# Kernel tuning notes

Hardware: AMD Instinct MI355X
Metric: run time of the kernel (lower is better)

Reference implementation:

```python
import jax, jax.numpy as jnp
import numpy as np

B, S, IN_DIM, P_DIM, H = 2, 2048, 1024, 512, 8
HD = P_DIM // H
N_PENTA = 1024
SCALES = (128, 256, 512)
K_NEIGH = max(16, min(int(S * 0.15), 128))  # adaptive window -> 128
SCALE = 1.0 / float(np.sqrt(HD))
EPS = 1e-5


def _ln(x, g, b):
    mu = jnp.mean(x, axis=-1, keepdims=True)
    var = jnp.mean((x - mu) ** 2, axis=-1, keepdims=True)
    return (x - mu) * jax.lax.rsqrt(var + EPS) * g + b


def setup_inputs() -> dict:
    key = jax.random.key(0)
    ks = list(jax.random.split(key, 6 + 2 * len(SCALES)))
    w = lambda k, shp: jax.random.normal(k, shp, jnp.float32) * 0.02
    inp = {
        'sequence_features': jax.random.normal(ks[0], (B, S, IN_DIM), jnp.float32),
        'shared_pentachora': jax.random.normal(ks[1], (N_PENTA, 5, P_DIM), jnp.float32),
        'shared_positions': jax.random.uniform(ks[2], (N_PENTA,), dtype=jnp.float32),
        'proj_W': w(ks[3], (IN_DIM, P_DIM)), 'proj_b': jnp.zeros((P_DIM,), jnp.float32),
        'ln_g': jnp.ones((P_DIM,), jnp.float32), 'ln_b': jnp.zeros((P_DIM,), jnp.float32),
        'qkv_W': w(ks[4], (P_DIM, 3 * P_DIM)), 'qkv_b': jnp.zeros((3 * P_DIM,), jnp.float32),
        'out_W': w(ks[5], (P_DIM, P_DIM)), 'out_b': jnp.zeros((P_DIM,), jnp.float32),
    }
    i = 6
    for s in SCALES:
        inp[f'w1_{s}'] = w(ks[i], (P_DIM, 2 * s)); inp[f'b1_{s}'] = jnp.zeros((2 * s,), jnp.float32)
        inp[f'g_{s}'] = jnp.ones((2 * s,), jnp.float32); inp[f'bb_{s}'] = jnp.zeros((2 * s,), jnp.float32)
        inp[f'w2_{s}'] = w(ks[i + 1], (2 * s, s)); inp[f'b2_{s}'] = jnp.zeros((s,), jnp.float32)
        i += 2
    return inp


def _attend_one(z_b, pos_b, qkv_W, qkv_b, out_W, out_b):
    # z_b: [S, P_DIM], pos_b: [S]
    qkv = (z_b @ qkv_W + qkv_b).reshape(S, 3, H, HD)
    q = jnp.transpose(qkv[:, 0], (1, 0, 2))  # [H, S, HD]
    k = jnp.transpose(qkv[:, 1], (1, 0, 2))
    v = jnp.transpose(qkv[:, 2], (1, 0, 2))
    dist = jnp.abs(pos_b[:, None] - pos_b[None, :])  # [S, S]
    _, routes = jax.lax.top_k(-dist, K_NEIGH)        # [S, K] nearest in Cantor space
    kg = k[:, routes, :]  # [H, S, K, HD] gathered keys
    vg = v[:, routes, :]
    scores = jnp.einsum('hqd,hqkd->hqk', q, kg) * SCALE
    attn = jax.nn.softmax(scores, axis=-1)
    out = jnp.einsum('hqk,hqkd->hqd', attn, vg)
    out = jnp.transpose(out, (1, 0, 2)).reshape(S, P_DIM)
    return out @ out_W + out_b


def reference(sequence_features, shared_pentachora, shared_positions, proj_W, proj_b, ln_g, ln_b, qkv_W, qkv_b, out_W, out_b, w1_128, b1_128, g_128, bb_128, w2_128, b2_128, w1_256, b1_256, g_256, bb_256, w2_256, b2_256, w1_512, b1_512, g_512, bb_512, w2_512, b2_512):
    # centroids from pentachora vertices, L2-normalized
    cent = shared_pentachora.mean(axis=1)
    cent = cent / jnp.clip(jnp.linalg.norm(cent, axis=-1, keepdims=True), 1e-12)
    # input projection -> LN -> GELU -> L2 normalize
    z = jax.nn.gelu(_ln(sequence_features @ proj_W + proj_b, ln_g, ln_b), approximate=False)
    z = z / jnp.clip(jnp.linalg.norm(z, axis=-1, keepdims=True), 1e-12)
    # match to opinion anchors, inherit Cantor positions
    anchor_ids = jnp.argmax(jnp.einsum('bnd,pd->bnp', z, cent), axis=-1)  # [B, S]
    cantor_positions = shared_positions[anchor_ids]  # [B, S]
    # per-sample geometric sparse attention (vmapped over batch)
    z_att = jax.vmap(_attend_one, in_axes=(0, 0, None, None, None, None))(
        z, cantor_positions, qkv_W, qkv_b, out_W, out_b)  # [B, S, P_DIM]
    pooled = z_att.mean(axis=1)  # [B, P_DIM] (no attention mask)
    scale_params = (
        (w1_128, b1_128, g_128, bb_128, w2_128, b2_128),
        (w1_256, b1_256, g_256, bb_256, w2_256, b2_256),
        (w1_512, b1_512, g_512, bb_512, w2_512, b2_512),
    )
    outs = []
    for (w1, b1, g, bb, w2, b2) in scale_params:
        h = jax.nn.gelu(_ln(pooled @ w1 + b1, g, bb), approximate=False)
        outs.append(h @ w2 + b2)
    return jnp.concatenate(outs, axis=-1)  # [B, 128+256+512] concatenated scale opinions
```

## Files before the change

### kernel.cpp

```cpp
#include <hip/hip_runtime.h>
#include <math.h>

#define DEV __device__ __forceinline__

static constexpr int S_LEN  = 2048;
static constexpr int IN_DIM = 1024;
static constexpr int P_DIM  = 512;
static constexpr int NHEAD  = 8;
static constexpr int HD     = 64;
static constexpr int KN     = 128;

typedef __attribute__((ext_vector_type(8))) short bf16x8;
typedef __attribute__((ext_vector_type(4))) float f32x4;

DEV float gelu_exact(float x) {
    return 0.5f * x * (1.0f + erff(x * 0.70710678118654752440f));
}

DEV short bf_hi(float x) {
    unsigned u = __float_as_uint(x);
    unsigned r = (u + 0x7fffu + ((u >> 16) & 1u)) >> 16;
    return (short)r;
}
DEV float bf_f(short h) { return __uint_as_float(((unsigned)(unsigned short)h) << 16); }

DEV float block_reduce_sum(float v, float* sm4) {
    #pragma unroll
    for (int off = 32; off; off >>= 1) v += __shfl_down(v, off, 64);
    int lane = threadIdx.x & 63, w = threadIdx.x >> 6;
    __syncthreads();
    if (lane == 0) sm4[w] = v;
    __syncthreads();
    return sm4[0] + sm4[1] + sm4[2] + sm4[3];
}

__global__ __launch_bounds__(256) void k_cent(const float* __restrict__ penta,
                                              short* __restrict__ ch,
                                              short* __restrict__ cl) {
    int p = blockIdx.x, t = threadIdx.x;
    __shared__ float sm4[4];
    float c0 = 0.f, c1 = 0.f;
    #pragma unroll
    for (int v = 0; v < 5; v++) {
        const float* row = penta + ((long)p * 5 + v) * P_DIM;
        c0 += row[t];
        c1 += row[t + 256];
    }
    c0 /= 5.0f; c1 /= 5.0f;
    float tot = block_reduce_sum(c0 * c0 + c1 * c1, sm4);
    float n = fmaxf(sqrtf(tot), 1e-12f);
    float v0 = c0 / n, v1 = c1 / n;
    short h0 = bf_hi(v0), h1 = bf_hi(v1);
    ch[p * P_DIM + t]       = h0;
    ch[p * P_DIM + t + 256] = h1;
    cl[p * P_DIM + t]       = bf_hi(v0 - bf_f(h0));
    cl[p * P_DIM + t + 256] = bf_hi(v1 - bf_f(h1));
}

template <int K, int N>
__global__ __launch_bounds__(256) void k_wt(const float* __restrict__ W,
                                            short* __restrict__ WTh,
                                            short* __restrict__ WTl) {
    __shared__ float tile[64][65];
    int bk = blockIdx.x, bn = blockIdx.y;
    int t = threadIdx.x;
    int c = t & 63, r4 = t >> 6;
    #pragma unroll
    for (int i = 0; i < 16; i++) {
        int row = r4 + i * 4;
        tile[row][c] = W[(long)(bk * 64 + row) * N + bn * 64 + c];
    }
    __syncthreads();
    #pragma unroll
    for (int i = 0; i < 16; i++) {
        int n = r4 + i * 4;
        float v = tile[c][n];
        short h = bf_hi(v);
        long o = (long)(bn * 64 + n) * K + bk * 64 + c;
        WTh[o] = h;
        WTl[o] = bf_hi(v - bf_f(h));
    }
}

template <int BM, int K, int N, int EPI, bool SPLITA>
__global__ __launch_bounds__(256) void k_mm(const float* __restrict__ Af,
                                            const short* __restrict__ Ash,
                                            const short* __restrict__ Asl,
                                            const short* __restrict__ BTh,
                                            const short* __restrict__ BTl,
                                            const float* __restrict__ bias,
                                            float* __restrict__ C,
                                            unsigned long long* __restrict__ rowkey) {
    constexpr int TI = BM / 32;
    __shared__ short Ah[BM * 40], Al[BM * 40], Bh[128 * 40], Bl[128 * 40];
    int t = threadIdx.x;
    int lane = t & 63, wave = t >> 6;
    int wr = (wave >> 1) * (BM / 2), wc = (wave & 1) * 64;
    int m = lane & 15, quad = lane >> 4;
    int rb = blockIdx.x * BM, cb = blockIdx.y * 128;

    f32x4 acc[TI][4];
    #pragma unroll
    for (int i = 0; i < TI; i++)
        #pragma unroll
        for (int j = 0; j < 4; j++) acc[i][j] = (f32x4){0.f, 0.f, 0.f, 0.f};

    for (int k0 = 0; k0 < K; k0 += 32) {
        __syncthreads();
        if constexpr (SPLITA) {
            #pragma unroll
            for (int ps = 0; ps < BM / 64; ps++) {
                int idx = t + ps * 256;
                int row = idx >> 2, c4 = idx & 3;
                *(float4*)(Ah + row * 40 + c4 * 8) =
                    *(const float4*)(Ash + (long)(rb + row) * K + k0 + c4 * 8);
                *(float4*)(Al + row * 40 + c4 * 8) =
                    *(const float4*)(Asl + (long)(rb + row) * K + k0 + c4 * 8);
            }
        } else {
            #pragma unroll
            for (int ps = 0; ps < BM / 32; ps++) {
                int row = (t >> 3) + ps * 32;
                int seg = t & 7;
                float4 v = *(const float4*)(Af + (long)(rb + row) * K + k0 + seg * 4);
                short h0 = bf_hi(v.x), h1 = bf_hi(v.y), h2 = bf_hi(v.z), h3 = bf_hi(v.w);
                short l0 = bf_hi(v.x - bf_f(h0)), l1 = bf_hi(v.y - bf_f(h1));
                short l2 = bf_hi(v.z - bf_f(h2)), l3 = bf_hi(v.w - bf_f(h3));
                *(short4*)(Ah + row * 40 + seg * 4) = make_short4(h0, h1, h2, h3);
                *(short4*)(Al + row * 40 + seg * 4) = make_short4(l0, l1, l2, l3);
            }
        }
        #pragma unroll
        for (int ps = 0; ps < 2; ps++) {
            int row = (t >> 2) + ps * 64;
            int seg = t & 3;
            *(float4*)(Bh + row * 40 + seg * 8) =
                *(const float4*)(BTh + (long)(cb + row) * K + k0 + seg * 8);
            *(float4*)(Bl + row * 40 + seg * 8) =
                *(const float4*)(BTl + (long)(cb + row) * K + k0 + seg * 8);
        }
        __syncthreads();

        bf16x8 ah[TI], al[TI], bh[4], bl[4];
        #pragma unroll
        for (int i = 0; i < TI; i++) {
            ah[i] = *(const bf16x8*)(Ah + (wr + i * 16 + m) * 40 + quad * 8);
            al[i] = *(const bf16x8*)(Al + (wr + i * 16 + m) * 40 + quad * 8);
        }
        #pragma unroll
        for (int j = 0; j < 4; j++) {
            bh[j] = *(const bf16x8*)(Bh + (wc + j * 16 + m) * 40 + quad * 8);
            bl[j] = *(const bf16x8*)(Bl + (wc + j * 16 + m) * 40 + quad * 8);
        }
        #pragma unroll
        for (int i = 0; i < TI; i++)
            #pragma unroll
            for (int j = 0; j < 4; j++) {
                acc[i][j] = __builtin_amdgcn_mfma_f32_16x16x32_bf16(ah[i], bh[j], acc[i][j], 0, 0, 0);
                acc[i][j] = __builtin_amdgcn_mfma_f32_16x16x32_bf16(ah[i], bl[j], acc[i][j], 0, 0, 0);
                acc[i][j] = __builtin_amdgcn_mfma_f32_16x16x32_bf16(al[i], bh[j], acc[i][j], 0, 0, 0);
            }
    }

    if (EPI == 0) {
        #pragma unroll
        for (int i = 0; i < TI; i++) {
            int gr0 = rb + wr + i * 16 + quad * 4;
            #pragma unroll
            for (int j = 0; j < 4; j++) {
                int gc = cb + wc + j * 16 + m;
                float bv = bias[gc];
                #pragma unroll
                for (int r = 0; r < 4; r++)
                    C[(long)(gr0 + r) * N + gc] = acc[i][j][r] + bv;
            }
        }
    } else {
        #pragma unroll
        for (int i = 0; i < TI; i++) {
            #pragma unroll
            for (int r = 0; r < 4; r++) {
                int gr = rb + wr + i * 16 + quad * 4 + r;
                float bv = acc[i][0][r];
                int bp = cb + wc + m;
                #pragma unroll
                for (int j = 1; j < 4; j++) {
                    float v = acc[i][j][r];
                    int p = cb + wc + j * 16 + m;
                    if (v > bv) { bv = v; bp = p; }
                }
                #pragma unroll
                for (int off = 1; off < 16; off <<= 1) {
                    float ov = __shfl_xor(bv, off, 64);
                    int op = __shfl_xor(bp, off, 64);
                    if (ov > bv || (ov == bv && op < bp)) { bv = ov; bp = op; }
                }
                if (m == 0) {
                    unsigned u = __float_as_uint(bv);
                    u = (u & 0x80000000u) ? ~u : (u | 0x80000000u);
                    unsigned long long key =
                        ((unsigned long long)u << 32) | (unsigned)(0xFFFFFFFFu - (unsigned)bp);
                    atomicMax(&rowkey[gr], key);
                }
            }
        }
    }
}

__global__ __launch_bounds__(256) void k_ln_gelu_norm(const float* __restrict__ Zin,
                                                      const float* __restrict__ g,
                                                      const float* __restrict__ b,
                                                      short* __restrict__ z_h,
                                                      short* __restrict__ z_l) {
    long row = blockIdx.x;
    int t = threadIdx.x;
    __shared__ float sm4[4];
    float x0 = Zin[row * P_DIM + t], x1 = Zin[row * P_DIM + t + 256];
    float mu = block_reduce_sum(x0 + x1, sm4) * (1.0f / P_DIM);
    float d0 = x0 - mu, d1 = x1 - mu;
    float var = block_reduce_sum(d0 * d0 + d1 * d1, sm4) * (1.0f / P_DIM);
    float rs = 1.0f / sqrtf(var + 1e-5f);
    float y0 = gelu_exact(d0 * rs * g[t] + b[t]);
    float y1 = gelu_exact(d1 * rs * g[t + 256] + b[t + 256]);
    float nn = block_reduce_sum(y0 * y0 + y1 * y1, sm4);
    float n = fmaxf(sqrtf(nn), 1e-12f);
    float v0 = y0 / n, v1 = y1 / n;
    short h0 = bf_hi(v0), h1 = bf_hi(v1);
    z_h[row * P_DIM + t]       = h0;
    z_h[row * P_DIM + t + 256] = h1;
    z_l[row * P_DIM + t]       = bf_hi(v0 - bf_f(h0));
    z_l[row * P_DIM + t + 256] = bf_hi(v1 - bf_f(h1));
}

__global__ __launch_bounds__(256) void k_sort(const unsigned long long* __restrict__ rowkey,
                                              const float* __restrict__ spos,
                                              int* __restrict__ order,
                                              float* __restrict__ pos_srt) {
    int b = blockIdx.x, t = threadIdx.x;
    __shared__ unsigned long long key[2048];
    for (int u = 0; u < 8; u++) {
        int i = t + u * 256;
        unsigned p = 0xFFFFFFFFu - (unsigned)(rowkey[b * 2048 + i] & 0xFFFFFFFFull);
        float pv = spos[p];
        key[i] = (((unsigned long long)__float_as_uint(pv)) << 32) | (unsigned)i;
    }
    __syncthreads();
    for (int k = 2; k <= 2048; k <<= 1) {
        for (int j = k >> 1; j > 0; j >>= 1) {
            for (int u = 0; u < 8; u++) {
                int i = t + u * 256;
                int l = i ^ j;
                if (l > i) {
                    bool up = ((i & k) == 0);
                    unsigned long long a = key[i], c = key[l];
                    if ((a > c) == up) { key[i] = c; key[l] = a; }
                }
            }
            __syncthreads();
        }
    }
    for (int u = 0; u < 8; u++) {
        int r = t + u * 256;
        unsigned long long kk = key[r];
        order[b * 2048 + r]   = (int)(kk & 0xffffffffu);
        pos_srt[b * 2048 + r] = __uint_as_float((unsigned)(kk >> 32));
    }
}

__global__ __launch_bounds__(256) void k_routes(const float* __restrict__ pos_srt,
                                                const int* __restrict__ order,
                                                unsigned long long* __restrict__ bmG,
                                                uint2* __restrict__ bounds) {
    int blk = blockIdx.x;
    int b = blk >> 9;
    int t = threadIdx.x;
    int lane = t & 63, wave = t >> 6;
    int r = (blk & 511) * 4 + wave;
    __shared__ float ps[2048];
    __shared__ unsigned short tk[2048];
    for (int u = 0; u < 8; u++) {
        int i = t + u * 256;
        ps[i] = pos_srt[b * 2048 + i];
        tk[i] = (unsigned short)order[b * 2048 + i];
    }
    __syncthreads();

    float pi = ps[r];
    float T = 3e38f;
    #pragma unroll
    for (int a2 = 0; a2 < 2; a2++) {
        int a = lane + a2 * 64;
        int jl = r - a, jr = r + 127 - a;
        if (jl >= 0 && jr <= 2047) {
            float dl = (a > 0)   ? (pi - ps[jl]) : 0.f;
            float dr = (a < 127) ? (ps[jr] - pi) : 0.f;
            T = fminf(T, fmaxf(dl, dr));
        }
    }
    #pragma unroll
    for (int off = 1; off < 64; off <<= 1) T = fminf(T, __shfl_xor(T, off, 64));

    int lo = 0, hi = r;
    while (lo < hi) { int mid = (lo + hi) >> 1; if (pi - ps[mid] <= T) hi = mid; else lo = mid + 1; }
    int mn = lo;
    lo = r; hi = 2047;
    while (lo < hi) { int mid = (lo + hi + 1) >> 1; if (ps[mid] - pi <= T) lo = mid; else hi = mid - 1; }
    int mx = lo;
    int Ls, Rs;
    if (T > 0.f) {
        lo = 0; hi = r;
        while (lo < hi) { int mid = (lo + hi) >> 1; if (pi - ps[mid] < T) hi = mid; else lo = mid + 1; }
        Ls = lo;
        lo = r; hi = 2047;
        while (lo < hi) { int mid = (lo + hi + 1) >> 1; if (ps[mid] - pi < T) lo = mid; else hi = mid - 1; }
        Rs = lo;
    } else { Ls = r + 1; Rs = r - 1; }

    int cnt_strict = (Rs >= Ls) ? (Rs - Ls + 1) : 0;
    int need = 128 - cnt_strict;
    int l0a, l0b, r0a, r0b;
    if (cnt_strict > 0) { l0a = mn; l0b = Ls - 1; r0a = Rs + 1; r0b = mx; }
    else                { l0a = mn; l0b = mx;     r0a = 1;      r0b = 0; }
    int nL = (l0b >= l0a) ? (l0b - l0a + 1) : 0;
    int nR = (r0b >= r0a) ? (r0b - r0a + 1) : 0;
    int tiecount = nL + nR;

    int X = 65535;
    if (need < tiecount) {
        int lo2 = 0, hi2 = 2047;
        while (lo2 < hi2) {
            int mid = (lo2 + hi2) >> 1;
            int cnt = 0;
            for (int e = lane; e < tiecount; e += 64) {
                int j = (e < nL) ? (l0a + e) : (r0a + e - nL);
                cnt += (tk[j] <= mid) ? 1 : 0;
            }
            #pragma unroll
            for (int off = 1; off < 64; off <<= 1) cnt += __shfl_xor(cnt, off, 64);
            if (cnt >= need) hi2 = mid; else lo2 = mid + 1;
        }
        X = lo2;
    }

    int qlo_loc = 1 << 30, qhi_loc = -1;
    if (lane < 32) {
        unsigned long long bits = 0;
        int j0 = lane << 6, j1 = j0 + 63;
        if (cnt_strict > 0) {
            int a0 = max(Ls, j0), a1 = min(Rs, j1);
            if (a0 <= a1) {
                int s = a0 - j0, e = a1 - j0;
                unsigned long long msk = (e - s == 63) ? ~0ull
                                       : (((1ull << (e - s + 1)) - 1) << s);
                bits |= msk;
            }
        }
        int a0 = max(l0a, j0), a1 = min(l0b, j1);
        for (int j = a0; j <= a1; j++) if (tk[j] <= X) bits |= 1ull << (j - j0);
        a0 = max(r0a, j0); a1 = min(r0b, j1);
        for (int j = a0; j <= a1; j++) if (tk[j] <= X) bits |= 1ull << (j - j0);
        if (bits) {
            qlo_loc = j0 + __builtin_ctzll(bits);
            qhi_loc = j0 + 63 - __builtin_clzll(bits);
        }
        bmG[((long)(b * 2048 + r)) * 32 + lane] = bits;
    }
    #pragma unroll
    for (int off = 1; off < 64; off <<= 1) {
        qlo_loc = min(qlo_loc, __shfl_xor(qlo_loc, off, 64));
        qhi_loc = max(qhi_loc, __shfl_xor(qhi_loc, off, 64));
    }
    if (lane == 0)
        bounds[b * 2048 + r] = make_uint2((unsigned)qlo_loc, (unsigned)qhi_loc);
}

__global__ __launch_bounds__(256) void k_kprep(const float* __restrict__ qkv,
                                               const int* __restrict__ order,
                                               short* __restrict__ Ks_h,
                                               short* __restrict__ Ks_l) {
    int b = blockIdx.y;
    int t = threadIdx.x;
    int lr = t >> 5;
    int seg = t & 31;
    int rank = blockIdx.x * 8 + lr;
    int tok = order[b * 2048 + rank];
    const float4* src = (const float4*)qkv + (long)(b * 2048 + tok) * 384 + 128 + seg * 4;
    long dsto = (long)(b * 2048 + rank) * 512 + seg * 16;
    #pragma unroll
    for (int u = 0; u < 4; u++) {
        float4 v = src[u];
        short h0 = bf_hi(v.x), h1 = bf_hi(v.y), h2 = bf_hi(v.z), h3 = bf_hi(v.w);
        *(short4*)(Ks_h + dsto + u * 4) = make_short4(h0, h1, h2, h3);
        *(short4*)(Ks_l + dsto + u * 4) =
            make_short4(bf_hi(v.x - bf_f(h0)), bf_hi(v.y - bf_f(h1)),
                        bf_hi(v.z - bf_f(h2)), bf_hi(v.w - bf_f(h3)));
    }
}

__global__ __launch_bounds__(256) void k_vprep(const float* __restrict__ qkv,
                                               const int* __restrict__ order,
                                               short* __restrict__ Vt_h) {
    __shared__ short tile[64][72];
    int rt = blockIdx.x, dt = blockIdx.y, b = blockIdx.z;
    int t = threadIdx.x;
    int lr = t >> 2;
    int q4 = t & 3;
    int tok = order[b * 2048 + rt * 64 + lr];
    const float4* src = (const float4*)qkv + (long)(b * 2048 + tok) * 384 + 256 + dt * 16;
    #pragma unroll
    for (int u = 0; u < 4; u++) {
        float4 v = src[q4 + u * 4];
        int d0 = (q4 + u * 4) * 4;
        tile[d0 + 0][lr] = bf_hi(v.x);
        tile[d0 + 1][lr] = bf_hi(v.y);
        tile[d0 + 2][lr] = bf_hi(v.z);
        tile[d0 + 3][lr] = bf_hi(v.w);
    }
    __syncthreads();
    int d = t >> 2, c4 = t & 3;
    long o = ((long)(b * 512 + dt * 64 + d)) * 2048 + rt * 64 + c4 * 16;
    #pragma unroll
    for (int j = 0; j < 4; j++)
        *(short4*)(Vt_h + o + j * 4) = make_short4(tile[d][c4 * 16 + j * 4 + 0],
                                                   tile[d][c4 * 16 + j * 4 + 1],
                                                   tile[d][c4 * 16 + j * 4 + 2],
                                                   tile[d][c4 * 16 + j * 4 + 3]);
}

__global__ __launch_bounds__(256) void k_attn(const float* __restrict__ qkv,
                                              const int* __restrict__ order,
                                              const unsigned long long* __restrict__ bmG,
                                              const uint2* __restrict__ bounds,
                                              const short* __restrict__ Ks_h,
                                              const short* __restrict__ Ks_l,
                                              const short* __restrict__ Vt_h,
                                              short* __restrict__ attn_h,
                                              short* __restrict__ attn_l) {
    __shared__ __align__(16) char smem[17024];
    short* Pt = (short*)smem;
    unsigned short* cm = (unsigned short*)(smem + 10240);
    float* Opart = (float*)smem;
    float2* ml = (float2*)(smem + 16384);
    int* sh_tok = (int*)(smem + 16896);
    int* sh_lohi = (int*)(smem + 16960);

    int gb = blockIdx.x;
    int b  = gb >> 9;
    int qg = (gb >> 2) & 127;
    int hp = gb & 3;
    int h0 = hp * 2;
    int r0 = qg * 16;
    int t = threadIdx.x;
    int lane = t & 63, wave = t >> 6;
    int rh = wave & 1, hs = wave >> 1;
    int key = lane & 15, quad = lane >> 4;

    const float4* qkvF4 = (const float4*)qkv;

    if (t < 16) sh_tok[t] = order[b * 2048 + r0 + t];
    if (t == 0) { sh_lohi[0] = 1 << 30; sh_lohi[1] = 0; }
    #pragma unroll
    for (int u = 0; u < 8; u++) {
        int e = t + u * 256;
        int c = e >> 4, q = e & 15;
        cm[c * 16 + q] = (unsigned short)(
            (bmG[((long)(b * 2048 + r0 + q)) * 32 + (c >> 2)] >> ((c & 3) * 16)) & 0xFFFF);
    }
    __syncthreads();
    if (t < 16) {
        uint2 bd = bounds[b * 2048 + r0 + t];
        atomicMin(&sh_lohi[0], (int)bd.x);
        atomicMax(&sh_lohi[1], (int)bd.y);
    }

    bf16x8 qh[2], ql[2];
    {
        long tq = (long)(b * 2048 + sh_tok[key]) * 384;
        #pragma unroll
        for (int ks = 0; ks < 2; ks++) {
            float4 v0 = qkvF4[tq + (h0 + hs) * 16 + ks * 8 + quad * 2];
            float4 v1 = qkvF4[tq + (h0 + hs) * 16 + ks * 8 + quad * 2 + 1];
            float vv[8] = {v0.x, v0.y, v0.z, v0.w, v1.x, v1.y, v1.z, v1.w};
            #pragma unroll
            for (int j = 0; j < 8; j++) {
                short hb = bf_hi(vv[j]);
                qh[ks][j] = hb;
                ql[ks][j] = bf_hi(vv[j] - bf_f(hb));
            }
        }
    }
    __syncthreads();
    int lo = sh_lohi[0] & ~63, hi = sh_lohi[1] + 1;

    float mrow[4], lrow[4];
    f32x4 Ont[4];
    #pragma unroll
    for (int r = 0; r < 4; r++) { mrow[r] = -1e30f; lrow[r] = 0.f; }
    #pragma unroll
    for (int nt = 0; nt < 4; nt++) Ont[nt] = (f32x4){0.f, 0.f, 0.f, 0.f};

    short* PtH = Pt + wave * 1280;
    short* PtL = PtH + 640;

    int hd = h0 + hs;
    long kbase = ((long)b * 2048) * 512 + hd * 64 + quad * 8;
    long vbase = ((long)(b * 512 + hd * 64 + key)) * 2048;

    for (int c0 = lo; c0 < hi; c0 += 64) {
        int cb = c0 + rh * 32;
        if (cb >= hi) continue;
        int ch0 = cb >> 4;
        unsigned long long m0 = *(const unsigned long long*)(cm + ch0 * 16 + quad * 4);
        unsigned long long m1 = (ch0 + 1 < 128)
            ? *(const unsigned long long*)(cm + (ch0 + 1) * 16 + quad * 4) : 0ull;
        if (!__any((m0 | m1) != 0ull)) continue;

        long kr0 = kbase + (long)(cb + key) * 512;
        long kr1 = kbase + (long)(cb + 16 + key) * 512;

        f32x4 S0 = (f32x4){0.f,0.f,0.f,0.f}, S1 = (f32x4){0.f,0.f,0.f,0.f};
        #pragma unroll
        for (int ks = 0; ks < 2; ks++) {
            bf16x8 b0h = *(const bf16x8*)(Ks_h + kr0 + ks * 32);
            bf16x8 b0l = *(const bf16x8*)(Ks_l + kr0 + ks * 32);
            bf16x8 b1h = *(const bf16x8*)(Ks_h + kr1 + ks * 32);
            bf16x8 b1l = *(const bf16x8*)(Ks_l + kr1 + ks * 32);
            S0 = __builtin_amdgcn_mfma_f32_16x16x32_bf16(qh[ks], b0h, S0, 0, 0, 0);
            S0 = __builtin_amdgcn_mfma_f32_16x16x32_bf16(qh[ks], b0l, S0, 0, 0, 0);
            S0 = __builtin_amdgcn_mfma_f32_16x16x32_bf16(ql[ks], b0h, S0, 0, 0, 0);
            S1 = __builtin_amdgcn_mfma_f32_16x16x32_bf16(qh[ks], b1h, S1, 0, 0, 0);
            S1 = __builtin_amdgcn_mfma_f32_16x16x32_bf16(qh[ks], b1l, S1, 0, 0, 0);
            S1 = __builtin_amdgcn_mfma_f32_16x16x32_bf16(ql[ks], b1h, S1, 0, 0, 0);
        }
        float s0[4], s1[4], p0[4], p1[4];
        unsigned bit0[4], bit1[4];
        #pragma unroll
        for (int r = 0; r < 4; r++) {
            bit0[r] = (unsigned)((m0 >> (r * 16 + key)) & 1);
            bit1[r] = (unsigned)((m1 >> (r * 16 + key)) & 1);
            s0[r] = bit0[r] ? S0[r] * 0.125f : -1e30f;
            s1[r] = bit1[r] ? S1[r] * 0.125f : -1e30f;
        }
        #pragma unroll
        for (int r = 0; r < 4; r++) {
            float cmax = fmaxf(s0[r], s1[r]);
            cmax = fmaxf(cmax, __shfl_xor(cmax, 1, 64));
            cmax = fmaxf(cmax, __shfl_xor(cmax, 2, 64));
            cmax = fmaxf(cmax, __shfl_xor(cmax, 4, 64));
            cmax = fmaxf(cmax, __shfl_xor(cmax, 8, 64));
            float mn = fmaxf(mrow[r], cmax);
            float alpha = __expf(mrow[r] - mn);
            mrow[r] = mn;
            p0[r] = bit0[r] ? __expf(s0[r] - mn) : 0.f;
            p1[r] = bit1[r] ? __expf(s1[r] - mn) : 0.f;
            float rs = p0[r] + p1[r];
            rs += __shfl_xor(rs, 1, 64);
            rs += __shfl_xor(rs, 2, 64);
            rs += __shfl_xor(rs, 4, 64);
            rs += __shfl_xor(rs, 8, 64);
            lrow[r] = lrow[r] * alpha + rs;
            #pragma unroll
            for (int nt = 0; nt < 4; nt++) Ont[nt][r] *= alpha;
        }
        #pragma unroll
        for (int r = 0; r < 4; r++) {
            short ha = bf_hi(p0[r]);
            PtH[(quad * 4 + r) * 40 + key] = ha;
            PtL[(quad * 4 + r) * 40 + key] = bf_hi(p0[r] - bf_f(ha));
            short hb = bf_hi(p1[r]);
            PtH[(quad * 4 + r) * 40 + 16 + key] = hb;
            PtL[(quad * 4 + r) * 40 + 16 + key] = bf_hi(p1[r] - bf_f(hb));
        }
        bf16x8 pfh = *(const bf16x8*)(PtH + key * 40 + quad * 8);
        bf16x8 pfl = *(const bf16x8*)(PtL + key * 40 + quad * 8);
        #pragma unroll
        for (int nt = 0; nt < 4; nt++) {
            bf16x8 vf = *(const bf16x8*)(Vt_h + vbase + (long)nt * 16 * 2048
                                         + cb + quad * 8);
            Ont[nt] = __builtin_amdgcn_mfma_f32_16x16x32_bf16(pfh, vf, Ont[nt], 0, 0, 0);
            Ont[nt] = __builtin_amdgcn_mfma_f32_16x16x32_bf16(pfl, vf, Ont[nt], 0, 0, 0);
        }
    }

    if (key == 0) {
        #pragma unroll
        for (int r = 0; r < 4; r++)
            ml[(rh * 2 + hs) * 16 + quad * 4 + r] = make_float2(mrow[r], lrow[r]);
    }
    __syncthreads();
    #pragma unroll
    for (int nt = 0; nt < 4; nt++)
        #pragma unroll
        for (int r = 0; r < 4; r++)
            Opart[rh * 2048 + (quad * 4 + r) * 128 + hs * 64 + nt * 16 + key] = Ont[nt][r];
    __syncthreads();

    {
        int q = t >> 4, hs2 = (t >> 3) & 1, ds = t & 7;
        float2 a = ml[(0 * 2 + hs2) * 16 + q];
        float2 c = ml[(1 * 2 + hs2) * 16 + q];
        float M = fmaxf(a.x, c.x);
        float w0 = __expf(a.x - M), w1 = __expf(c.x - M);
        float denom = a.y * w0 + c.y * w1;
        float inv = 1.0f / fmaxf(denom, 1e-37f);
        long off = (long)(b * 2048 + sh_tok[q]) * P_DIM + (h0 + hs2) * HD + ds * 8;
        short hsv[8], lsv[8];
        #pragma unroll
        for (int j = 0; j < 8; j++) {
            int d = hs2 * 64 + ds * 8 + j;
            float o = (Opart[q * 128 + d] * w0 + Opart[2048 + q * 128 + d] * w1) * inv;
            hsv[j] = bf_hi(o);
            lsv[j] = bf_hi(o - bf_f(hsv[j]));
        }
        *(short4*)(attn_h + off)     = make_short4(hsv[0], hsv[1], hsv[2], hsv[3]);
        *(short4*)(attn_h + off + 4) = make_short4(hsv[4], hsv[5], hsv[6], hsv[7]);
        *(short4*)(attn_l + off)     = make_short4(lsv[0], lsv[1], lsv[2], lsv[3]);
        *(short4*)(attn_l + off + 4) = make_short4(lsv[4], lsv[5], lsv[6], lsv[7]);
    }
}

__global__ __launch_bounds__(256) void k_pool(const float* __restrict__ zatt,
                                              float* __restrict__ pooled) {
    int b = blockIdx.y, chunk = blockIdx.x, t = threadIdx.x;
    float a0 = 0.f, a1 = 0.f;
    for (int s = 0; s < 16; s++) {
        long row = ((long)b * S_LEN + chunk * 16 + s) * P_DIM;
        a0 += zatt[row + t];
        a1 += zatt[row + t + 256];
    }
    atomicAdd(&pooled[b * P_DIM + t], a0);
    atomicAdd(&pooled[b * P_DIM + t + 256], a1);
}

__global__ __launch_bounds__(256) void k_exp_fc1(const float* __restrict__ pooled,
                                                 const float* __restrict__ w1_0, const float* __restrict__ b1_0,
                                                 const float* __restrict__ w1_1, const float* __restrict__ b1_1,
                                                 const float* __restrict__ w1_2, const float* __restrict__ b1_2,
                                                 float* __restrict__ h) {
    int t = threadIdx.x, b = blockIdx.y;
    int c = blockIdx.x * 256 + t;
    __shared__ float pl[P_DIM];
    pl[t]       = pooled[b * P_DIM + t]       * (1.0f / S_LEN);
    pl[t + 256] = pooled[b * P_DIM + t + 256] * (1.0f / S_LEN);
    __syncthreads();

    const float* wp; const float* bp; int s2, j;
    if (c < 256)      { wp = w1_0; bp = b1_0; s2 = 256;  j = c; }
    else if (c < 768) { wp = w1_1; bp = b1_1; s2 = 512;  j = c - 256; }
    else              { wp = w1_2; bp = b1_2; s2 = 1024; j = c - 768; }

    const float* p = wp + j;
    float acc = 0.f;
    #pragma unroll 16
    for (int k = 0; k < P_DIM; k++) {
        acc = fmaf(pl[k], *p, acc);
        p += s2;
    }
    h[(long)b * 1792 + c] = acc + bp[j];
}

__global__ __launch_bounds__(256) void k_exp_ln(float* __restrict__ h,
                                                const float* __restrict__ g0, const float* __restrict__ bb0,
                                                const float* __restrict__ g1, const float* __restrict__ bb1,
                                                const float* __restrict__ g2, const float* __restrict__ bb2) {
    int e = blockIdx.x, b = blockIdx.y, t = threadIdx.x;
    __shared__ float sm4[4];
    const int offs[3] = {0, 256, 768};
    const int ns[3]   = {256, 512, 1024};
    const float* gs[3]  = {g0, g1, g2};
    const float* bbs[3] = {bb0, bb1, bb2};
    int n = ns[e];
    float* hp = h + (long)b * 1792 + offs[e];
    const float* g = gs[e]; const float* bb = bbs[e];

    float x[4];
    float loc = 0.f;
    for (int u = 0; u < 4; u++) {
        int j = t + u * 256;
        x[u] = (j < n) ? hp[j] : 0.f;
        loc += x[u];
    }
    float mu = block_reduce_sum(loc, sm4) / (float)n;
    loc = 0.f;
    for (int u = 0; u < 4; u++) {
        int j = t + u * 256;
        if (j < n) { float d = x[u] - mu; loc += d * d; }
    }
    float var = block_reduce_sum(loc, sm4) / (float)n;
    float rs = 1.0f / sqrtf(var + 1e-5f);
    for (int u = 0; u < 4; u++) {
        int j = t + u * 256;
        if (j < n) hp[j] = gelu_exact((x[u] - mu) * rs * g[j] + bb[j]);
    }
}

__global__ __launch_bounds__(256) void k_exp_fc2(const float* __restrict__ h,
                                                 const float* __restrict__ w2_0, const float* __restrict__ b2_0,
                                                 const float* __restrict__ w2_1, const float* __restrict__ b2_1,
                                                 const float* __restrict__ w2_2, const float* __restrict__ b2_2,
                                                 float* __restrict__ out) {
    int t = threadIdx.x, b = blockIdx.y;
    int c = blockIdx.x * 256 + t;
    __shared__ float hs[1792];
    for (int u = 0; u < 7; u++) hs[t + u * 256] = h[(long)b * 1792 + t + u * 256];
    __syncthreads();
    if (c >= 896) return;

    const float* wp; const float* bp; int s2, sN, j, off_h;
    if (c < 128)      { wp = w2_0; bp = b2_0; s2 = 256;  sN = 128; j = c;       off_h = 0; }
    else if (c < 384) { wp = w2_1; bp = b2_1; s2 = 512;  sN = 256; j = c - 128; off_h = 256; }
    else              { wp = w2_2; bp = b2_2; s2 = 1024; sN = 512; j = c - 384; off_h = 768; }

    const float* p = wp + j;
    const float* hh = hs + off_h;
    float acc = 0.f;
    #pragma unroll 16
    for (int k = 0; k < s2; k++) {
        acc = fmaf(hh[k], *p, acc);
        p += sN;
    }
    out[b * 896 + c] = acc + bp[j];
}

extern "C" void kernel_launch(void* const* d_in, const int* in_sizes, int n_in,
                              void* d_out, int out_size, void* d_ws, size_t ws_size,
                              hipStream_t stream) {
    const float* seq   = (const float*)d_in[0];
    const float* penta = (const float*)d_in[1];
    const float* spos  = (const float*)d_in[2];
    const float* projW = (const float*)d_in[3];
    const float* projb = (const float*)d_in[4];
    const float* lng   = (const float*)d_in[5];
    const float* lnb   = (const float*)d_in[6];
    const float* qkvW  = (const float*)d_in[7];
    const float* qkvb  = (const float*)d_in[8];
    const float* outW  = (const float*)d_in[9];
    const float* outb  = (const float*)d_in[10];

    float* ws      = (float*)d_ws;
    float* z_pre   = ws;
    short* z_h     = (short*)(z_pre + 2097152);
    short* z_l     = z_h + 2097152;
    float* qkv     = (float*)(z_l + 2097152);
    float* pos     = qkv + 6291456;
    float* pooled  = pos + 4096;
    float* hbuf    = pooled + 1024;
    unsigned long long* rowkey = (unsigned long long*)(hbuf + 4096);
    float* pos_srt = (float*)(rowkey + 4096);
    int*   order   = (int*)(pos_srt + 4096);
    uint2* bounds  = (uint2*)(order + 4096);
    unsigned long long* bmG = (unsigned long long*)(bounds + 4096);
    short* cent_h  = (short*)(bmG + 131072);
    short* cent_l  = cent_h + 524288;
    short* pjWT_h  = cent_l + 524288;
    short* pjWT_l  = pjWT_h + 524288;
    short* qkWT_h  = pjWT_l + 524288;
    short* qkWT_l  = qkWT_h + 786432;
    short* owWT_h  = qkWT_l + 786432;
    short* owWT_l  = owWT_h + 262144;
    short* attn_h  = z_h;
    short* attn_l  = z_l;
    float* zatt    = z_pre;

    short* Ks_h = (short*)z_pre;
    short* Ks_l = Ks_h + 2097152;
    short* Vt_h = cent_h;

    k_cent<<<1024, 256, 0, stream>>>(penta, cent_h, cent_l);
    { dim3 g(16, 8);  k_wt<IN_DIM, P_DIM><<<g, 256, 0, stream>>>(projW, pjWT_h, pjWT_l); }
    { dim3 g(8, 24);  k_wt<P_DIM, 3 * P_DIM><<<g, 256, 0, stream>>>(qkvW, qkWT_h, qkWT_l); }
    { dim3 g(8, 8);   k_wt<P_DIM, P_DIM><<<g, 256, 0, stream>>>(outW, owWT_h, owWT_l); }

    { dim3 g(64, 4);  k_mm<64, IN_DIM, P_DIM, 0, false><<<g, 256, 0, stream>>>(
          seq, nullptr, nullptr, pjWT_h, pjWT_l, projb, z_pre, nullptr); }
    k_ln_gelu_norm<<<4096, 256, 0, stream>>>(z_pre, lng, lnb, z_h, z_l);

    hipMemsetAsync(rowkey, 0, 4096 * sizeof(unsigned long long), stream);
    { dim3 g(64, 8);  k_mm<64, P_DIM, 1024, 1, true><<<g, 256, 0, stream>>>(
          nullptr, z_h, z_l, cent_h, cent_l, nullptr, nullptr, rowkey); }
    k_sort<<<2, 256, 0, stream>>>(rowkey, spos, order, pos_srt);

    { dim3 g(64, 12); k_mm<64, P_DIM, 3 * P_DIM, 0, true><<<g, 256, 0, stream>>>(
          nullptr, z_h, z_l, qkWT_h, qkWT_l, qkvb, qkv, nullptr); }
    k_routes<<<1024, 256, 0, stream>>>(pos_srt, order, bmG, bounds);
    { dim3 g(256, 2); k_kprep<<<g, 256, 0, stream>>>(qkv, order, Ks_h, Ks_l); }
    { dim3 g(32, 8, 2); k_vprep<<<g, 256, 0, stream>>>(qkv, order, Vt_h); }
    k_attn<<<1024, 256, 0, stream>>>(qkv, order, bmG, bounds,
                                     Ks_h, Ks_l, Vt_h, attn_h, attn_l);
    { dim3 g(64, 4);  k_mm<64, P_DIM, P_DIM, 0, true><<<g, 256, 0, stream>>>(
          nullptr, attn_h, attn_l, owWT_h, owWT_l, outb, zatt, nullptr); }

    hipMemsetAsync(pooled, 0, 1024 * sizeof(float), stream);
    { dim3 pg(128, 2); k_pool<<<pg, 256, 0, stream>>>(zatt, pooled); }

    dim3 g1(7, 2);
    k_exp_fc1<<<g1, 256, 0, stream>>>(pooled,
        (const float*)d_in[11], (const float*)d_in[12],
        (const float*)d_in[17], (const float*)d_in[18],
        (const float*)d_in[23], (const float*)d_in[24], hbuf);
    dim3 g2(3, 2);
    k_exp_ln<<<g2, 256, 0, stream>>>(hbuf,
        (const float*)d_in[13], (const float*)d_in[14],
        (const float*)d_in[19], (const float*)d_in[20],
        (const float*)d_in[25], (const float*)d_in[26]);
    dim3 g3(4, 2);
    k_exp_fc2<<<g3, 256, 0, stream>>>(hbuf,
        (const float*)d_in[15], (const float*)d_in[16],
        (const float*)d_in[21], (const float*)d_in[22],
        (const float*)d_in[27], (const float*)d_in[28], (float*)d_out);
}
```

Baseline: 401.8 us.

## Pool attention output before out-projection, shrink GEMM tiles, widen sort block

Uses linearity of the mean: the attention kernel now sums its per-token outputs per head straight into a pooled buffer with atomics, and a small kernel applies out_W and S·out_b to the pooled vector. This removes the full out-projection GEMM, the out_W transpose/split kernel, the attn hi/lo stores and the pooling kernel. GEMMs switch from 64- to 32-row tiles to launch more blocks, and the bitonic sort runs with 1024 threads instead of 256. The pooled sum is accumulated in fp32 via atomics, so summation order and rounding differ from the reference.

```diff
diff --git a/kernel.cpp b/kernel.cpp
--- a/kernel.cpp
+++ b/kernel.cpp
@@ -91,7 +91,7 @@
                                             const float* __restrict__ bias,
                                             float* __restrict__ C,
                                             unsigned long long* __restrict__ rowkey) {
-    constexpr int TI = BM / 32;
+    constexpr int TI = (BM + 31) / 32;
     __shared__ short Ah[BM * 40], Al[BM * 40], Bh[128 * 40], Bl[128 * 40];
     int t = threadIdx.x;
     int lane = t & 63, wave = t >> 6;
@@ -108,14 +108,17 @@
     for (int k0 = 0; k0 < K; k0 += 32) {
         __syncthreads();
         if constexpr (SPLITA) {
+            constexpr int TOT = BM * 4;
             #pragma unroll
-            for (int ps = 0; ps < BM / 64; ps++) {
+            for (int ps = 0; ps < (TOT + 255) / 256; ps++) {
                 int idx = t + ps * 256;
-                int row = idx >> 2, c4 = idx & 3;
-                *(float4*)(Ah + row * 40 + c4 * 8) =
-                    *(const float4*)(Ash + (long)(rb + row) * K + k0 + c4 * 8);
-                *(float4*)(Al + row * 40 + c4 * 8) =
-                    *(const float4*)(Asl + (long)(rb + row) * K + k0 + c4 * 8);
+                if (idx < TOT) {
+                    int row = idx >> 2, c4 = idx & 3;
+                    *(float4*)(Ah + row * 40 + c4 * 8) =
+                        *(const float4*)(Ash + (long)(rb + row) * K + k0 + c4 * 8);
+                    *(float4*)(Al + row * 40 + c4 * 8) =
+                        *(const float4*)(Asl + (long)(rb + row) * K + k0 + c4 * 8);
+                }
             }
         } else {
             #pragma unroll
@@ -232,14 +235,14 @@
     z_l[row * P_DIM + t + 256] = bf_hi(v1 - bf_f(h1));
 }
 
-__global__ __launch_bounds__(256) void k_sort(const unsigned long long* __restrict__ rowkey,
-                                              const float* __restrict__ spos,
-                                              int* __restrict__ order,
-                                              float* __restrict__ pos_srt) {
+__global__ __launch_bounds__(1024) void k_sort(const unsigned long long* __restrict__ rowkey,
+                                               const float* __restrict__ spos,
+                                               int* __restrict__ order,
+                                               float* __restrict__ pos_srt) {
     int b = blockIdx.x, t = threadIdx.x;
     __shared__ unsigned long long key[2048];
-    for (int u = 0; u < 8; u++) {
-        int i = t + u * 256;
+    for (int u = 0; u < 2; u++) {
+        int i = t + u * 1024;
         unsigned p = 0xFFFFFFFFu - (unsigned)(rowkey[b * 2048 + i] & 0xFFFFFFFFull);
         float pv = spos[p];
         key[i] = (((unsigned long long)__float_as_uint(pv)) << 32) | (unsigned)i;
@@ -247,8 +250,8 @@
     __syncthreads();
     for (int k = 2; k <= 2048; k <<= 1) {
         for (int j = k >> 1; j > 0; j >>= 1) {
-            for (int u = 0; u < 8; u++) {
-                int i = t + u * 256;
+            for (int u = 0; u < 2; u++) {
+                int i = t + u * 1024;
                 int l = i ^ j;
                 if (l > i) {
                     bool up = ((i & k) == 0);
@@ -259,8 +262,8 @@
             __syncthreads();
         }
     }
-    for (int u = 0; u < 8; u++) {
-        int r = t + u * 256;
+    for (int u = 0; u < 2; u++) {
+        int r = t + u * 1024;
         unsigned long long kk = key[r];
         order[b * 2048 + r]   = (int)(kk & 0xffffffffu);
         pos_srt[b * 2048 + r] = __uint_as_float((unsigned)(kk >> 32));
@@ -434,15 +437,15 @@
                                               const short* __restrict__ Ks_h,
                                               const short* __restrict__ Ks_l,
                                               const short* __restrict__ Vt_h,
-                                              short* __restrict__ attn_h,
-                                              short* __restrict__ attn_l) {
-    __shared__ __align__(16) char smem[17024];
+                                              float* __restrict__ pooledZ) {
+    __shared__ __align__(16) char smem[17280];
     short* Pt = (short*)smem;
     unsigned short* cm = (unsigned short*)(smem + 10240);
     float* Opart = (float*)smem;
     float2* ml = (float2*)(smem + 16384);
     int* sh_tok = (int*)(smem + 16896);
     int* sh_lohi = (int*)(smem + 16960);
+    float2* sc = (float2*)(smem + 16968);
 
     int gb = blockIdx.x;
     int b  = gb >> 9;
@@ -593,43 +596,44 @@
         #pragma unroll
         for (int r = 0; r < 4; r++)
             Opart[rh * 2048 + (quad * 4 + r) * 128 + hs * 64 + nt * 16 + key] = Ont[nt][r];
-    __syncthreads();
-
-    {
-        int q = t >> 4, hs2 = (t >> 3) & 1, ds = t & 7;
+
+    if (t < 32) {
+        int q = t >> 1, hs2 = t & 1;
         float2 a = ml[(0 * 2 + hs2) * 16 + q];
         float2 c = ml[(1 * 2 + hs2) * 16 + q];
         float M = fmaxf(a.x, c.x);
         float w0 = __expf(a.x - M), w1 = __expf(c.x - M);
-        float denom = a.y * w0 + c.y * w1;
-        float inv = 1.0f / fmaxf(denom, 1e-37f);
-        long off = (long)(b * 2048 + sh_tok[q]) * P_DIM + (h0 + hs2) * HD + ds * 8;
-        short hsv[8], lsv[8];
-        #pragma unroll
-        for (int j = 0; j < 8; j++) {
-            int d = hs2 * 64 + ds * 8 + j;
-            float o = (Opart[q * 128 + d] * w0 + Opart[2048 + q * 128 + d] * w1) * inv;
-            hsv[j] = bf_hi(o);
-            lsv[j] = bf_hi(o - bf_f(hsv[j]));
-        }
-        *(short4*)(attn_h + off)     = make_short4(hsv[0], hsv[1], hsv[2], hsv[3]);
-        *(short4*)(attn_h + off + 4) = make_short4(hsv[4], hsv[5], hsv[6], hsv[7]);
-        *(short4*)(attn_l + off)     = make_short4(lsv[0], lsv[1], lsv[2], lsv[3]);
-        *(short4*)(attn_l + off + 4) = make_short4(lsv[4], lsv[5], lsv[6], lsv[7]);
-    }
-}
-
-__global__ __launch_bounds__(256) void k_pool(const float* __restrict__ zatt,
-                                              float* __restrict__ pooled) {
-    int b = blockIdx.y, chunk = blockIdx.x, t = threadIdx.x;
-    float a0 = 0.f, a1 = 0.f;
-    for (int s = 0; s < 16; s++) {
-        long row = ((long)b * S_LEN + chunk * 16 + s) * P_DIM;
-        a0 += zatt[row + t];
-        a1 += zatt[row + t + 256];
-    }
-    atomicAdd(&pooled[b * P_DIM + t], a0);
-    atomicAdd(&pooled[b * P_DIM + t + 256], a1);
+        float inv = 1.0f / fmaxf(a.y * w0 + c.y * w1, 1e-37f);
+        sc[hs2 * 16 + q] = make_float2(w0 * inv, w1 * inv);
+    }
+    __syncthreads();
+
+    if (t < 128) {
+        int d = t, hs2 = d >> 6;
+        float s = 0.f;
+        #pragma unroll
+        for (int q = 0; q < 16; q++) {
+            float2 w = sc[hs2 * 16 + q];
+            s += Opart[q * 128 + d] * w.x + Opart[2048 + q * 128 + d] * w.y;
+        }
+        atomicAdd(&pooledZ[b * P_DIM + h0 * HD + d], s);
+    }
+}
+
+__global__ __launch_bounds__(256) void k_opool(const float* __restrict__ pooledZ,
+                                               const float* __restrict__ outW,
+                                               const float* __restrict__ outb,
+                                               float* __restrict__ pooled) {
+    int b = blockIdx.y, t = threadIdx.x;
+    int c = blockIdx.x * 256 + t;
+    __shared__ float pz[P_DIM];
+    pz[t]       = pooledZ[b * P_DIM + t];
+    pz[t + 256] = pooledZ[b * P_DIM + t + 256];
+    __syncthreads();
+    float acc = 0.f;
+    #pragma unroll 8
+    for (int d = 0; d < P_DIM; d++) acc = fmaf(pz[d], outW[d * P_DIM + c], acc);
+    pooled[b * P_DIM + c] = acc + (float)S_LEN * outb[c];
 }
 
 __global__ __launch_bounds__(256) void k_exp_fc1(const float* __restrict__ pooled,
@@ -742,8 +746,8 @@
     short* z_h     = (short*)(z_pre + 2097152);
     short* z_l     = z_h + 2097152;
     float* qkv     = (float*)(z_l + 2097152);
-    float* pos     = qkv + 6291456;
-    float* pooled  = pos + 4096;
+    float* pooledZ = qkv + 6291456;
+    float* pooled  = pooledZ + 4096;
     float* hbuf    = pooled + 1024;
     unsigned long long* rowkey = (unsigned long long*)(hbuf + 4096);
     float* pos_srt = (float*)(rowkey + 4096);
@@ -756,11 +760,6 @@
     short* pjWT_l  = pjWT_h + 524288;
     short* qkWT_h  = pjWT_l + 524288;
     short* qkWT_l  = qkWT_h + 786432;
-    short* owWT_h  = qkWT_l + 786432;
-    short* owWT_l  = owWT_h + 262144;
-    short* attn_h  = z_h;
-    short* attn_l  = z_l;
-    float* zatt    = z_pre;
 
     short* Ks_h = (short*)z_pre;
     short* Ks_l = Ks_h + 2097152;
@@ -769,29 +768,26 @@
     k_cent<<<1024, 256, 0, stream>>>(penta, cent_h, cent_l);
     { dim3 g(16, 8);  k_wt<IN_DIM, P_DIM><<<g, 256, 0, stream>>>(projW, pjWT_h, pjWT_l); }
     { dim3 g(8, 24);  k_wt<P_DIM, 3 * P_DIM><<<g, 256, 0, stream>>>(qkvW, qkWT_h, qkWT_l); }
-    { dim3 g(8, 8);   k_wt<P_DIM, P_DIM><<<g, 256, 0, stream>>>(outW, owWT_h, owWT_l); }
-
-    { dim3 g(64, 4);  k_mm<64, IN_DIM, P_DIM, 0, false><<<g, 256, 0, stream>>>(
+
+    { dim3 g(128, 4); k_mm<32, IN_DIM, P_DIM, 0, false><<<g, 256, 0, stream>>>(
           seq, nullptr, nullptr, pjWT_h, pjWT_l, projb, z_pre, nullptr); }
     k_ln_gelu_norm<<<4096, 256, 0, stream>>>(z_pre, lng, lnb, z_h, z_l);
 
     hipMemsetAsync(rowkey, 0, 4096 * sizeof(unsigned long long), stream);
-    { dim3 g(64, 8);  k_mm<64, P_DIM, 1024, 1, true><<<g, 256, 0, stream>>>(
+    hipMemsetAsync(pooledZ, 0, 1024 * sizeof(float), stream);
+    { dim3 g(128, 8); k_mm<32, P_DIM, 1024, 1, true><<<g, 256, 0, stream>>>(
           nullptr, z_h, z_l, cent_h, cent_l, nullptr, nullptr, rowkey); }
-    k_sort<<<2, 256, 0, stream>>>(rowkey, spos, order, pos_srt);
-
-    { dim3 g(64, 12); k_mm<64, P_DIM, 3 * P_DIM, 0, true><<<g, 256, 0, stream>>>(
+    k_sort<<<2, 1024, 0, stream>>>(rowkey, spos, order, pos_srt);
+
+    { dim3 g(128, 12); k_mm<32, P_DIM, 3 * P_DIM, 0, true><<<g, 256, 0, stream>>>(
           nullptr, z_h, z_l, qkWT_h, qkWT_l, qkvb, qkv, nullptr); }
     k_routes<<<1024, 256, 0, stream>>>(pos_srt, order, bmG, bounds);
     { dim3 g(256, 2); k_kprep<<<g, 256, 0, stream>>>(qkv, order, Ks_h, Ks_l); }
     { dim3 g(32, 8, 2); k_vprep<<<g, 256, 0, stream>>>(qkv, order, Vt_h); }
     k_attn<<<1024, 256, 0, stream>>>(qkv, order, bmG, bounds,
-                                     Ks_h, Ks_l, Vt_h, attn_h, attn_l);
-    { dim3 g(64, 4);  k_mm<64, P_DIM, P_DIM, 0, true><<<g, 256, 0, stream>>>(
-          nullptr, attn_h, attn_l, owWT_h, owWT_l, outb, zatt, nullptr); }
-
-    hipMemsetAsync(pooled, 0, 1024 * sizeof(float), stream);
-    { dim3 pg(128, 2); k_pool<<<pg, 256, 0, stream>>>(zatt, pooled); }
+                                     Ks_h, Ks_l, Vt_h, pooledZ);
+
+    { dim3 g(2, 2); k_opool<<<g, 256, 0, stream>>>(pooledZ, outW, outb, pooled); }
 
     dim3 g1(7, 2);
     k_exp_fc1<<<g1, 256, 0, stream>>>(pooled,
```

Result: faster. 393.0 us (-2.2%).
